# Optimization experiments

Measured on AMD Instinct MI355X. Metric: run time of the kernel, lower is better.

The kernel has to match this reference:

```python
import jax, jax.numpy as jnp
import numpy as np
from jax import lax

NDF = 128
OUT_CH = 256
N_INPUT = 4096
H = W = 64
A_FEAT = OUT_CH * 2 * 2   # 1024
B_OUT = OUT_CH            # 256
C_ROW = 16
BATCH = 128
EPS = 1e-5


def conv2d_s2(x, w):
    # x: NCHW, w: OIHW, stride 2, pad 1 (kernel 4) -> halves spatial dims
    return lax.conv_general_dilated(x, w, window_strides=(2, 2),
                                    padding=[(1, 1), (1, 1)],
                                    dimension_numbers=("NCHW", "OIHW", "NCHW"))


def batchnorm(x, gamma, beta):
    # training-mode batch stats over (N, H, W)
    mean = jnp.mean(x, axis=(0, 2, 3), keepdims=True)
    var = jnp.var(x, axis=(0, 2, 3), keepdims=True)
    xn = (x - mean) * lax.rsqrt(var + EPS)
    return xn * gamma[None, :, None, None] + beta[None, :, None, None]


def lrelu(x):
    return jnp.where(x >= 0, x, 0.2 * x)


def setup_inputs() -> dict:
    key = jax.random.key(0)
    ks = jax.random.split(key, 16)
    s = lambda fan: 1.0 / np.sqrt(fan)
    inp = {
        "image": jax.random.normal(ks[0], (BATCH, 3, H, W), jnp.float32),
        "word_vectors": jax.random.normal(ks[1], (BATCH, N_INPUT), jnp.float32),
        "fc_w": jax.random.normal(ks[2], (H * W, N_INPUT), jnp.float32) * s(N_INPUT),
        "w1": jax.random.normal(ks[3], (NDF, 4, 4, 4), jnp.float32) * s(4 * 16),
        "w2": jax.random.normal(ks[4], (NDF * 2, NDF, 4, 4), jnp.float32) * s(NDF * 16),
        "w3": jax.random.normal(ks[5], (NDF * 2, NDF * 2, 4, 4), jnp.float32) * s(NDF * 2 * 16),
        "w4": jax.random.normal(ks[6], (NDF * 4, NDF * 2, 4, 4), jnp.float32) * s(NDF * 2 * 16),
        "w5": jax.random.normal(ks[7], (OUT_CH, NDF * 4, 4, 4), jnp.float32) * s(NDF * 4 * 16),
        "g2": jnp.ones((NDF * 2,), jnp.float32),
        "b2": jnp.zeros((NDF * 2,), jnp.float32),
        "g3": jnp.ones((NDF * 2,), jnp.float32),
        "b3": jnp.zeros((NDF * 2,), jnp.float32),
        "g4": jnp.ones((NDF * 4,), jnp.float32),
        "b4": jnp.zeros((NDF * 4,), jnp.float32),
        "T": jax.random.uniform(ks[8], (A_FEAT, B_OUT, C_ROW), jnp.float32,
                                 minval=0.0, maxval=1.0 / A_FEAT),
    }
    return inp


def reference(image, word_vectors, fc_w, w1, w2, w3, w4, w5,
              g2, b2, g3, b3, g4, b4, T):
    b = image.shape[0]
    # fc: Linear(no bias) + ReLU (dropout = identity at p=0 / eval)
    wv = jax.nn.relu(word_vectors @ fc_w.T)            # [b, H*W]
    wv = wv.reshape(b, 1, H, W)
    x = jnp.concatenate([image, wv], axis=1)           # [b, 4, 64, 64]
    # conv stack (spectral norm acts on weights; raw weights used here)
    x = lrelu(conv2d_s2(x, w1))                        # [b, ndf, 32, 32]
    x = lrelu(batchnorm(conv2d_s2(x, w2), g2, b2))     # [b, 2ndf, 16, 16]
    x = lrelu(batchnorm(conv2d_s2(x, w3), g3, b3))     # [b, 2ndf, 8, 8]
    x = lrelu(batchnorm(conv2d_s2(x, w4), g4, b4))     # [b, 4ndf, 4, 4]
    x = conv2d_s2(x, w5)                               # [b, out_ch, 2, 2]
    # minibatch discrimination
    feat = x.reshape(b, A_FEAT)                        # [b, 1024]
    Ms = (feat @ T.reshape(A_FEAT, B_OUT * C_ROW)).reshape(b, B_OUT, C_ROW)
    # pairwise L1 over C, exp, sum over batch (including self, as in the loop)
    d = jnp.sum(jnp.abs(Ms[:, None, :, :] - Ms[None, :, :, :]), axis=-1)  # [b,b,B]
    mbd = jnp.sum(jnp.exp(-d), axis=1)                 # [b, B]
    return jnp.concatenate([feat, mbd], axis=1)        # [b, 1280]
```

## Files before the change

kernel.cpp:

```cpp
#include <hip/hip_runtime.h>
#include <cstddef>

#define BB 128

typedef unsigned short u16;
typedef __attribute__((ext_vector_type(8))) short short8;
typedef __attribute__((ext_vector_type(4))) short short4v;
typedef __attribute__((ext_vector_type(4))) float f32x4;

constexpr int ilog2c(int v){ return v<=1 ? 0 : 1+ilog2c(v>>1); }

__device__ __forceinline__ u16 f2b(float f){
  union {float f; unsigned u;} x; x.f = f;
  unsigned u = x.u + 0x7fffu + ((x.u>>16)&1u);
  return (u16)(u>>16);
}
__device__ __forceinline__ float b2f(u16 h){
  union {unsigned u; float f;} x; x.u = ((unsigned)h)<<16;
  return x.f;
}

#define GLOAD_LDS16(gsrc, ldsdst) \
  __builtin_amdgcn_global_load_lds((const __attribute__((address_space(1))) void*)(gsrc), \
      (__attribute__((address_space(3))) void*)(ldsdst), 16, 0, 0)

template<int IC, int OC, int OH, int STORE, int KSPLIT=1>
__global__ __launch_bounds__(512) void convmm2(
    const u16* __restrict__ xp, const u16* __restrict__ wtT, void* __restrict__ yv)
{
  constexpr int OW = OH, S = OH*OW;
  constexpr int IHp = 2*OH+2, IWp = 2*OW+2;
  constexpr int KT = 16*IC;
  constexpr int KTS = KT / KSPLIT;
  constexpr int NT = KTS / 64;
  constexpr int LS = ilog2c(S), LOW = ilog2c(OW), L4 = ilog2c(4*IC);
  __shared__ u16 As[2*128*64];
  __shared__ u16 Bs[2*128*64];
  const int tid = threadIdx.x;
  const int m0 = blockIdx.x*128;
  const int n0 = blockIdx.y*128;
  const int kbase = (KSPLIT>1) ? blockIdx.z*KTS : 0;
  const int wave = tid>>6, l = tid&63;
  const int wm = wave>>1, wn = wave&1;

  size_t abase[2]; int au[2];
  #pragma unroll
  for (int t=0;t<2;++t){
    int unit = tid + t*512;
    int r = unit>>3, us = unit&7;
    au[t] = us ^ (r&7);
    int p = m0 + r;
    int b = p >> LS, s = p & (S-1);
    int oh = s >> LOW, ow = s & (OW-1);
    abase[t] = ((size_t)(b*IHp + 2*oh)*IWp + 2*ow)*IC;
  }
  const u16* bsrc[2];
  #pragma unroll
  for (int t=0;t<2;++t){
    int unit = tid + t*512;
    int r = unit>>3, us = unit&7;
    bsrc[t] = wtT + (size_t)(n0+r)*KT + (size_t)(us ^ (r&7))*8;
  }

  auto stage = [&](int half, int k0){
    #pragma unroll
    for (int t=0;t<2;++t){
      int k = k0 + au[t]*8;
      int kh = k >> L4, koff = k & (4*IC-1);
      GLOAD_LDS16(xp + abase[t] + (size_t)kh*IWp*IC + koff,
                  &As[half*8192 + (size_t)(t*512 + wave*64)*8]);
    }
    #pragma unroll
    for (int t=0;t<2;++t){
      GLOAD_LDS16(bsrc[t] + k0, &Bs[half*8192 + (size_t)(t*512 + wave*64)*8]);
    }
  };

  f32x4 acc[2][4] = {};

  stage(0, kbase);
  __syncthreads();
  int cur = 0;
  for (int t=0; t<NT; ++t){
    if (t+1 < NT) stage(cur^1, kbase + (t+1)*64);
    #pragma unroll
    for (int kk=0;kk<2;++kk){
      short8 af[2], bfm[4];
      #pragma unroll
      for (int mi=0;mi<2;++mi){
        int row = wm*32 + mi*16 + (l&15);
        int u = (kk*4 + (l>>4)) ^ (row&7);
        af[mi] = *(const short8*)(&As[cur*8192 + row*64 + u*8]);
      }
      #pragma unroll
      for (int ni=0;ni<4;++ni){
        int row = wn*64 + ni*16 + (l&15);
        int u = (kk*4 + (l>>4)) ^ (row&7);
        bfm[ni] = *(const short8*)(&Bs[cur*8192 + row*64 + u*8]);
      }
      #pragma unroll
      for (int mi=0;mi<2;++mi)
        #pragma unroll
        for (int ni=0;ni<4;++ni)
          acc[mi][ni] = __builtin_amdgcn_mfma_f32_16x16x32_bf16(af[mi], bfm[ni], acc[mi][ni], 0,0,0);
    }
    __syncthreads();
    cur ^= 1;
  }
  #pragma unroll
  for (int mi=0;mi<2;++mi){
    #pragma unroll
    for (int ni=0;ni<4;++ni){
      #pragma unroll
      for (int r=0;r<4;++r){
        int row = m0 + wm*32 + mi*16 + (l>>4)*4 + r;
        int col = n0 + wn*64 + ni*16 + (l&15);
        float v = acc[mi][ni][r];
        if (STORE==0){
          ((u16*)yv)[(size_t)row*OC + col] = f2b(v);
        } else if (STORE==1){
          v = v>=0.f ? v : 0.2f*v;
          int b = row>>LS, s = row&(S-1);
          int oh = s>>LOW, ow = s&(OW-1);
          ((u16*)yv)[((size_t)(b*(OH+2) + oh+1)*(OW+2) + ow+1)*OC + col] = f2b(v);
        } else {
          ((float*)yv)[((size_t)blockIdx.z*(BB*S) + row)*OC + col] = v;
        }
      }
    }
  }
}

template<int B_FP32>
__global__ __launch_bounds__(256) void gemm128_split(
    const u16* __restrict__ A, const void* __restrict__ Bsrc,
    float* __restrict__ part, int K, int kchunk)
{
  __shared__ u16 As[2*128*64];
  __shared__ u16 Bs[2*64*64];
  const int tid = threadIdx.x;
  const int n0 = blockIdx.x*64;
  const int kbase = blockIdx.y*kchunk;
  const int wave = tid>>6, l = tid&63;
  const u16* asrc[4];
  #pragma unroll
  for (int t=0;t<4;++t){
    int unit = tid + t*256, r = unit>>3, us = unit&7;
    asrc[t] = A + (size_t)r*K + (size_t)(us ^ (r&7))*8;
  }
  const float* bf32[4]; int bdst32[4];
  const u16* b16[2];
  if (B_FP32){
    const float* Bf = (const float*)Bsrc;
    #pragma unroll
    for (int t=0;t<4;++t){
      int unit = tid + t*256;
      int r = unit>>4, u4 = unit&15;
      int u = u4>>1, hf = u4&1;
      int us = u ^ (r&7);
      bf32[t] = Bf + (size_t)(n0+r)*K + u4*4;
      bdst32[t] = r*64 + us*8 + hf*4;
    }
  } else {
    const u16* Bb = (const u16*)Bsrc;
    #pragma unroll
    for (int t=0;t<2;++t){
      int unit = tid + t*256, r = unit>>3, us = unit&7;
      b16[t] = Bb + (size_t)(n0+r)*K + (size_t)(us ^ (r&7))*8;
    }
  }

  auto stageA = [&](int half, int k0){
    #pragma unroll
    for (int t=0;t<4;++t)
      GLOAD_LDS16(asrc[t] + k0, &As[half*8192 + (size_t)(t*256 + wave*64)*8]);
  };
  auto stageB16 = [&](int half, int k0){
    #pragma unroll
    for (int t=0;t<2;++t)
      GLOAD_LDS16(b16[t] + k0, &Bs[half*4096 + (size_t)(t*256 + wave*64)*8]);
  };
  float4 breg[4];
  auto loadB32 = [&](int k0){
    #pragma unroll
    for (int t=0;t<4;++t) breg[t] = *(const float4*)(bf32[t] + k0);
  };
  auto writeB32 = [&](int half){
    #pragma unroll
    for (int t=0;t<4;++t){
      short4v o; o[0]=(short)f2b(breg[t].x); o[1]=(short)f2b(breg[t].y);
      o[2]=(short)f2b(breg[t].z); o[3]=(short)f2b(breg[t].w);
      *(short4v*)(&Bs[half*4096 + bdst32[t]]) = o;
    }
  };

  f32x4 acc[2][4] = {};
  const int NT = kchunk >> 6;
  stageA(0, kbase);
  if (B_FP32){ loadB32(kbase); writeB32(0); } else stageB16(0, kbase);
  __syncthreads();
  int cur = 0;
  for (int t=0;t<NT;++t){
    const int k0 = kbase + t*64;
    if (t+1 < NT){
      stageA(cur^1, k0+64);
      if (B_FP32) loadB32(k0+64);
      else stageB16(cur^1, k0+64);
    }
    #pragma unroll
    for (int kk=0;kk<2;++kk){
      short8 af[2], bfm[4];
      #pragma unroll
      for (int mi=0;mi<2;++mi){
        int row = wave*32 + mi*16 + (l&15);
        int u = (kk*4 + (l>>4)) ^ (row&7);
        af[mi] = *(const short8*)(&As[cur*8192 + row*64 + u*8]);
      }
      #pragma unroll
      for (int ni=0;ni<4;++ni){
        int row = ni*16 + (l&15);
        int u = (kk*4 + (l>>4)) ^ (row&7);
        bfm[ni] = *(const short8*)(&Bs[cur*4096 + row*64 + u*8]);
      }
      #pragma unroll
      for (int mi=0;mi<2;++mi)
        #pragma unroll
        for (int ni=0;ni<4;++ni)
          acc[mi][ni] = __builtin_amdgcn_mfma_f32_16x16x32_bf16(af[mi], bfm[ni], acc[mi][ni], 0,0,0);
    }
    if (B_FP32 && t+1 < NT) writeB32(cur^1);
    __syncthreads();
    cur ^= 1;
  }
  #pragma unroll
  for (int mi=0;mi<2;++mi){
    #pragma unroll
    for (int ni=0;ni<4;++ni){
      #pragma unroll
      for (int r=0;r<4;++r){
        int m = wave*32 + mi*16 + (l>>4)*4 + r;
        int n = n0 + ni*16 + (l&15);
        part[((size_t)blockIdx.y*128 + m)*4096 + n] = acc[mi][ni][r];
      }
    }
  }
}

template<int Hp, int C>
__device__ __forceinline__ void zb_border(u16* __restrict__ buf, int idx, int count){
  if (idx >= count) return;
  constexpr int NP = 4*Hp - 4;
  constexpr int PC = NP*C;
  int b = idx / PC;
  int rem = idx - b*PC;
  int p = rem >> ilog2c(C);
  int c = rem & (C-1);
  int h, w;
  if (p < Hp){ h = 0; w = p; }
  else if (p < 2*Hp){ h = Hp-1; w = p - Hp; }
  else { int q = p - 2*Hp; h = 1 + (q>>1); w = (q&1) ? (Hp-1) : 0; }
  buf[(((size_t)b*Hp + h)*Hp + w)*C + c] = 0;
}

__global__ __launch_bounds__(256) void fc_reduce_zb(const float* __restrict__ part,
                                                    u16* __restrict__ xp0,
                                                    u16* __restrict__ xp1, u16* __restrict__ xp2)
{
  const int blk = blockIdx.x, tid = threadIdx.x;
  if (blk < 2048){
    int idx = blk*256 + tid;
    float s = 0.f;
    #pragma unroll
    for (int i=0;i<16;++i) s += part[(size_t)i*524288 + idx];
    float v = fmaxf(s, 0.f);
    int m = idx>>12, n = idx&4095;
    int h = n>>6, w2 = n&63;
    xp0[((size_t)(m*66 + h+1)*66 + w2+1)*4 + 3] = f2b(v);
  } else if (blk < 10496){
    zb_border<34,128>(xp1, (blk-2048)*256 + tid, 2162688);
  } else {
    zb_border<18,256>(xp2, (blk-10496)*256 + tid, 2228224);
  }
}

__global__ __launch_bounds__(256) void reduce_ms(const float* __restrict__ part, float* __restrict__ outv)
{
  int idx = blockIdx.x*256 + threadIdx.x;
  float s = 0.f;
  #pragma unroll
  for (int i=0;i<8;++i) s += part[(size_t)i*524288 + idx];
  outv[idx] = s;
}

template<int NS, int C>
__global__ __launch_bounds__(256) void reduce_bn(
    const float* __restrict__ part, u16* __restrict__ y,
    float* __restrict__ stats, int Mblk, int Mtot)
{
  constexpr int CU = C/8, NR = 256/CU, LCU = ilog2c(CU);
  __shared__ float red[NR*C];
  const int cu = threadIdx.x & (CU-1);
  const int rg = threadIdx.x >> LCU;
  const int base = blockIdx.x*Mblk;
  float s[8] = {}, ss[8] = {};
  for (int p = base+rg; p < base+Mblk; p += NR){
    float a8[8];
    #pragma unroll
    for (int j=0;j<8;++j) a8[j]=0.f;
    #pragma unroll
    for (int i=0;i<NS;++i){
      const float* src = part + ((size_t)i*Mtot + p)*C + cu*8;
      float4 v0 = *(const float4*)src;
      float4 v1 = *(const float4*)(src+4);
      a8[0]+=v0.x; a8[1]+=v0.y; a8[2]+=v0.z; a8[3]+=v0.w;
      a8[4]+=v1.x; a8[5]+=v1.y; a8[6]+=v1.z; a8[7]+=v1.w;
    }
    u16 o[8];
    #pragma unroll
    for (int j=0;j<8;++j){
      o[j] = f2b(a8[j]);
      float vb = b2f(o[j]);
      s[j]+=vb; ss[j]+=vb*vb;
    }
    *(short8*)(y + (size_t)p*C + cu*8) = *(short8*)o;
  }
  #pragma unroll
  for (int j=0;j<8;++j) red[rg*C + cu*8 + j] = s[j];
  __syncthreads();
  for (int c=threadIdx.x; c<C; c+=256){
    float t=0.f;
    #pragma unroll
    for (int r2=0;r2<NR;++r2) t += red[r2*C+c];
    stats[blockIdx.x*512 + c] = t;
  }
  __syncthreads();
  #pragma unroll
  for (int j=0;j<8;++j) red[rg*C + cu*8 + j] = ss[j];
  __syncthreads();
  for (int c=threadIdx.x; c<C; c+=256){
    float t=0.f;
    #pragma unroll
    for (int r2=0;r2<NR;++r2) t += red[r2*C+c];
    stats[131072 + blockIdx.x*512 + c] = t;
  }
}

__global__ __launch_bounds__(256) void conv5_reduce(const float* __restrict__ part,
                                                    float* __restrict__ out, u16* __restrict__ featb)
{
  int idx = blockIdx.x*256 + threadIdx.x;
  float s = 0.f;
  #pragma unroll
  for (int i=0;i<32;++i) s += part[(size_t)i*131072 + idx];
  int row = idx>>8, col = idx&255;
  int b = row>>2, sp = row&3;
  out[(size_t)b*1280 + col*4 + sp] = s;
  featb[(size_t)b*1024 + col*4 + sp] = f2b(s);
}

template<int IC, int ICP>
__device__ __forceinline__ void repack_dev(const float* __restrict__ w, u16* __restrict__ wt,
                                           int oc, int tid, float* ls){
  for (int i=tid; i<IC*16; i+=256){
    int ic = i>>4, khkw = i&15;
    ls[ic*17+khkw] = w[(size_t)oc*IC*16 + i];
  }
  __syncthreads();
  constexpr int KT = 16*ICP;
  constexpr int LP = ilog2c(ICP);
  for (int k=tid; k<KT; k+=256){
    int khkw = k >> LP, ic = k & (ICP-1);
    float v = (ic<IC) ? ls[ic*17+khkw] : 0.f;
    wt[(size_t)oc*KT + k] = f2b(v);
  }
}

__device__ __forceinline__ void transpose_dev(const float* __restrict__ T, u16* __restrict__ Tt,
                                              int idx, int tid, float* tile){
  int bx = idx & 127, by = idx >> 7;
  int kb = by*32, nb = bx*32;
  int tx = tid&31, ty = tid>>5;
  #pragma unroll
  for (int i=0;i<32;i+=8)
    tile[(ty+i)*33 + tx] = T[(size_t)(kb+ty+i)*4096 + nb+tx];
  __syncthreads();
  #pragma unroll
  for (int i=0;i<32;i+=8)
    Tt[(size_t)(nb+ty+i)*1024 + kb+tx] = f2b(tile[tx*33 + ty+i]);
}

__global__ __launch_bounds__(256) void prep_all(
    const float* __restrict__ w1, const float* __restrict__ w2, const float* __restrict__ w3,
    const float* __restrict__ w4, const float* __restrict__ w5, const float* __restrict__ T,
    const float* __restrict__ wvec, const float* __restrict__ img,
    u16* wt1T, u16* wt2T, u16* wt3T, u16* wt4T, u16* wt5T, u16* Tt, u16* wvb, u16* xp0)
{
  __shared__ float ls[512*17];
  const int blk = blockIdx.x, tid = threadIdx.x;
  if (blk < 128)        repack_dev<4,4>(w1, wt1T, blk, tid, ls);
  else if (blk < 384)   repack_dev<128,128>(w2, wt2T, blk-128, tid, ls);
  else if (blk < 640)   repack_dev<256,256>(w3, wt3T, blk-384, tid, ls);
  else if (blk < 1152)  repack_dev<256,256>(w4, wt4T, blk-640, tid, ls);
  else if (blk < 1408)  repack_dev<512,512>(w5, wt5T, blk-1152, tid, ls);
  else if (blk < 5504)  transpose_dev(T, Tt, blk-1408, tid, ls);
  else if (blk < 7552){ int i = (blk-5504)*256 + tid; wvb[i] = f2b(wvec[i]); }
  else if (blk < 9600){
    int idx = (blk-7552)*256 + tid;
    int b = idx>>12, s = idx&4095;
    int h = s>>6, w = s&63;
    short4v o;
    o[0] = (short)f2b(img[(size_t)(b*3+0)*4096 + s]);
    o[1] = (short)f2b(img[(size_t)(b*3+1)*4096 + s]);
    o[2] = (short)f2b(img[(size_t)(b*3+2)*4096 + s]);
    o[3] = 0;
    *(short4v*)(xp0 + ((size_t)(b*66 + h+1)*66 + w+1)*4) = o;
  } else {
    zb_border<66,4>(xp0, (blk-9600)*256 + tid, 133120);
  }
}

template<int C>
__global__ __launch_bounds__(256) void bn_stats2(const u16* __restrict__ y, float* __restrict__ stats, int Mblk){
  constexpr int CU = C/8, NR = 256/CU, LCU = ilog2c(CU);
  __shared__ float red[NR*C];
  const int cu = threadIdx.x & (CU-1);
  const int rg = threadIdx.x >> LCU;
  const int base = blockIdx.x*Mblk;
  float s[8] = {}, ss[8] = {};
  for (int p = base+rg; p < base+Mblk; p += NR){
    short8 v = *(const short8*)(y + (size_t)p*C + cu*8);
    #pragma unroll
    for (int j=0;j<8;++j){ float f=b2f((u16)v[j]); s[j]+=f; ss[j]+=f*f; }
  }
  #pragma unroll
  for (int j=0;j<8;++j) red[rg*C + cu*8 + j] = s[j];
  __syncthreads();
  for (int c=threadIdx.x; c<C; c+=256){
    float t=0.f;
    #pragma unroll
    for (int r2=0;r2<NR;++r2) t += red[r2*C+c];
    stats[blockIdx.x*512 + c] = t;
  }
  __syncthreads();
  #pragma unroll
  for (int j=0;j<8;++j) red[rg*C + cu*8 + j] = ss[j];
  __syncthreads();
  for (int c=threadIdx.x; c<C; c+=256){
    float t=0.f;
    #pragma unroll
    for (int r2=0;r2<NR;++r2) t += red[r2*C+c];
    stats[131072 + blockIdx.x*512 + c] = t;
  }
}

template<int C>
__global__ __launch_bounds__(C) void bn_finalize(float* __restrict__ stats, const float* __restrict__ g,
                                                 const float* __restrict__ be, float cnt){
  int c = threadIdx.x;
  float s=0.f, ss=0.f;
  for (int b=0;b<256;++b){ s += stats[b*512+c]; ss += stats[131072 + b*512+c]; }
  float m = s/cnt;
  float var = ss/cnt - m*m;
  float A = rsqrtf(var + 1e-5f)*g[c];
  stats[262144 + c] = A;
  stats[262144 + 512 + c] = be[c] - m*A;
}

template<int C, int OH>
__device__ __forceinline__ void bn_apply_body(const u16* __restrict__ y, const float* __restrict__ stats,
                                              u16* __restrict__ xp, int idx){
  constexpr int S = OH*OH, LS = ilog2c(S), LOW = ilog2c(OH);
  constexpr int CU = C/8, LCU = ilog2c(CU);
  int p = idx >> LCU, cu = idx & (CU-1);
  short8 v8 = *(const short8*)(y + (size_t)p*C + cu*8);
  const float* Ap = stats + 262144;
  const float* Bp = stats + 262144 + 512;
  u16 o[8];
  #pragma unroll
  for (int j=0;j<8;++j){
    float v = b2f((u16)v8[j])*Ap[cu*8+j] + Bp[cu*8+j];
    o[j] = f2b(v>=0.f ? v : 0.2f*v);
  }
  int b = p>>LS, s = p&(S-1), oh = s>>LOW, ow = s&(OH-1);
  *(short8*)(xp + ((size_t)(b*(OH+2)+oh+1)*(OH+2)+ow+1)*C + cu*8) = *(short8*)o;
}

template<int C, int OH>
__global__ __launch_bounds__(256) void bn_apply(const u16* __restrict__ y, const float* __restrict__ stats,
                                                u16* __restrict__ xp){
  bn_apply_body<C,OH>(y, stats, xp, blockIdx.x*256 + threadIdx.x);
}

__global__ __launch_bounds__(256) void bn_apply2_zb(const u16* __restrict__ y, const float* __restrict__ stats,
                                                    u16* __restrict__ xp, u16* xp3, u16* xp4){
  const int blk = blockIdx.x, tid = threadIdx.x;
  if (blk < 4096)       bn_apply_body<256,16>(y, stats, xp, blk*256 + tid);
  else if (blk < 8704)  zb_border<10,256>(xp3, (blk-4096)*256 + tid, 1179648);
  else                  zb_border<6,512>(xp4, (blk-8704)*256 + tid, 1310720);
}

__global__ __launch_bounds__(256) void mbd_part(const float* __restrict__ Ms, float* __restrict__ part)
{
  const int i = blockIdx.x;
  const int ch = blockIdx.y;
  const int o = threadIdx.x;
  float mi[16];
  #pragma unroll
  for (int u = 0; u < 4; ++u) {
    float4 v = *(const float4*)&Ms[(size_t)i * 4096 + o * 16 + u * 4];
    mi[u*4+0]=v.x; mi[u*4+1]=v.y; mi[u*4+2]=v.z; mi[u*4+3]=v.w;
  }
  float acc = 0.f;
  for (int j = ch*16; j < ch*16 + 16; ++j) {
    float d = 0.f;
    #pragma unroll
    for (int u = 0; u < 4; ++u) {
      float4 v = *(const float4*)&Ms[(size_t)j * 4096 + o * 16 + u * 4];
      d += fabsf(mi[u*4+0]-v.x) + fabsf(mi[u*4+1]-v.y) + fabsf(mi[u*4+2]-v.z) + fabsf(mi[u*4+3]-v.w);
    }
    acc += __expf(-d);
  }
  part[((size_t)ch*128 + i)*256 + o] = acc;
}

__global__ __launch_bounds__(256) void mbd_reduce(const float* __restrict__ part, float* __restrict__ out)
{
  int idx = blockIdx.x*256 + threadIdx.x;
  int i = idx>>8, o = idx&255;
  float s = 0.f;
  #pragma unroll
  for (int c=0;c<8;++c) s += part[((size_t)c*128 + i)*256 + o];
  out[(size_t)i*1280 + 1024 + o] = s;
}

__global__ void ws_too_small(float* out, int n){
  int idx = blockIdx.x*256+threadIdx.x;
  if (idx<n) out[idx] = -777.0f;
}

extern "C" void kernel_launch(void* const* d_in, const int* in_sizes, int n_in,
                              void* d_out, int out_size, void* d_ws, size_t ws_size,
                              hipStream_t stream)
{
  const float* image = (const float*)d_in[0];
  const float* wvec  = (const float*)d_in[1];
  const float* fc_w  = (const float*)d_in[2];
  const float* w1    = (const float*)d_in[3];
  const float* w2    = (const float*)d_in[4];
  const float* w3    = (const float*)d_in[5];
  const float* w4    = (const float*)d_in[6];
  const float* w5    = (const float*)d_in[7];
  const float* g2    = (const float*)d_in[8];
  const float* b2    = (const float*)d_in[9];
  const float* g3    = (const float*)d_in[10];
  const float* b3    = (const float*)d_in[11];
  const float* g4    = (const float*)d_in[12];
  const float* b4    = (const float*)d_in[13];
  const float* T     = (const float*)d_in[14];
  float* out = (float*)d_out;
  char* wsb = (char*)d_ws;

  const size_t NEED = 105816064ull;
  if (ws_size < NEED) {
    ws_too_small<<<(out_size + 255)/256, 256, 0, stream>>>(out, out_size);
    return;
  }

  u16* xp1   = (u16*)(wsb + 0);
  u16* y3    = (u16*)(wsb + 0);
  u16* xp3   = (u16*)(wsb + 4194304);
  u16* y4    = (u16*)(wsb + 10747904);
  u16* xp4   = (u16*)(wsb + 12845056);
  float* Ms  = (float*)(wsb + 17563648);
  u16* featb = (u16*)(wsb + 19660800);
  float* stats = (float*)(wsb + 19922944);
  u16* xp2   = (u16*)(wsb + 37879808);
  float* gpartF = (float*)(wsb + 37879808);
  float* c4part = (float*)(wsb + 37879808);
  float* c5part = (float*)(wsb + 37879808);
  float* mbdpart = (float*)(wsb + 37879808);
  u16* y2    = (u16*)(wsb + 59113472);
  float* gpartM = (float*)(wsb + 59113472);
  float* c3part = (float*)(wsb + 59113472);
  u16* xp0   = (u16*)(wsb + 75890688);
  u16* wt1T  = (u16*)(wsb + 84811776);
  u16* wt2T  = (u16*)(wsb + 84844544);
  u16* wt3T  = (u16*)(wsb + 85893120);
  u16* wt4T  = (u16*)(wsb + 87990272);
  u16* wt5T  = (u16*)(wsb + 92184576);
  u16* Tt    = (u16*)(wsb + 96378880);
  u16* wvb   = (u16*)(wsb + 104767488);

  prep_all<<<10120, 256, 0, stream>>>(w1, w2, w3, w4, w5, T, wvec, image,
                                      wt1T, wt2T, wt3T, wt4T, wt5T, Tt, wvb, xp0);

  gemm128_split<1><<<dim3(64,16), 256, 0, stream>>>(wvb, fc_w, gpartF, 4096, 256);
  fc_reduce_zb<<<19200, 256, 0, stream>>>(gpartF, xp0, xp1, xp2);

  convmm2<4,128,32,1><<<dim3(1024,1), 512, 0, stream>>>(xp0, wt1T, xp1);
  convmm2<128,256,16,0><<<dim3(256,2), 512, 0, stream>>>(xp1, wt2T, y2);

  bn_stats2<256><<<256, 256, 0, stream>>>(y2, stats, 128);
  bn_finalize<256><<<1, 256, 0, stream>>>(stats, g2, b2, 32768.f);
  bn_apply2_zb<<<13824, 256, 0, stream>>>(y2, stats, xp2, xp3, xp4);

  convmm2<256,256,8,3,2><<<dim3(64,2,2), 512, 0, stream>>>(xp2, wt3T, c3part);
  reduce_bn<2,256><<<256, 256, 0, stream>>>(c3part, y3, stats, 32, 8192);
  bn_finalize<256><<<1, 256, 0, stream>>>(stats, g3, b3, 8192.f);
  bn_apply<256,8><<<1024, 256, 0, stream>>>(y3, stats, xp3);

  convmm2<256,512,4,3,4><<<dim3(16,4,4), 512, 0, stream>>>(xp3, wt4T, c4part);
  reduce_bn<4,512><<<256, 256, 0, stream>>>(c4part, y4, stats, 8, 2048);
  bn_finalize<512><<<1, 512, 0, stream>>>(stats, g4, b4, 2048.f);
  bn_apply<512,4><<<512, 256, 0, stream>>>(y4, stats, xp4);

  convmm2<512,256,2,3,32><<<dim3(4,2,32), 512, 0, stream>>>(xp4, wt5T, c5part);
  conv5_reduce<<<512, 256, 0, stream>>>(c5part, out, featb);

  gemm128_split<0><<<dim3(64,8), 256, 0, stream>>>(featb, Tt, gpartM, 1024, 128);
  reduce_ms<<<2048, 256, 0, stream>>>(gpartM, Ms);

  mbd_part<<<dim3(128,8), 256, 0, stream>>>(Ms, mbdpart);
  mbd_reduce<<<128, 256, 0, stream>>>(mbdpart, out);
}
```

Before: 266.9 us.

## Store split-K partials in bf16 and fuse minibatch-discrimination reduction

Split-K partial sums from the fc GEMM and conv3/4/5 are written and read as bf16 instead of fp32, halving the traffic of these intermediate buffers. The two-kernel minibatch-discrimination part/reduce is merged into one kernel with 1024-thread blocks reducing through shared memory, removing a launch and a global round trip. Rounding partials to bf16 before summation adds accumulation error.

```diff
diff --git a/kernel.cpp b/kernel.cpp
--- a/kernel.cpp
+++ b/kernel.cpp
@@ -124,17 +124,17 @@
           int oh = s>>LOW, ow = s&(OW-1);
           ((u16*)yv)[((size_t)(b*(OH+2) + oh+1)*(OW+2) + ow+1)*OC + col] = f2b(v);
         } else {
-          ((float*)yv)[((size_t)blockIdx.z*(BB*S) + row)*OC + col] = v;
+          ((u16*)yv)[((size_t)blockIdx.z*(BB*S) + row)*OC + col] = f2b(v);
         }
       }
     }
   }
 }
 
-template<int B_FP32>
+template<int B_FP32, int P16>
 __global__ __launch_bounds__(256) void gemm128_split(
     const u16* __restrict__ A, const void* __restrict__ Bsrc,
-    float* __restrict__ part, int K, int kchunk)
+    void* __restrict__ part, int K, int kchunk)
 {
   __shared__ u16 As[2*128*64];
   __shared__ u16 Bs[2*64*64];
@@ -240,7 +240,9 @@
       for (int r=0;r<4;++r){
         int m = wave*32 + mi*16 + (l>>4)*4 + r;
         int n = n0 + ni*16 + (l&15);
-        part[((size_t)blockIdx.y*128 + m)*4096 + n] = acc[mi][ni][r];
+        size_t off = ((size_t)blockIdx.y*128 + m)*4096 + n;
+        if (P16) ((u16*)part)[off] = f2b(acc[mi][ni][r]);
+        else     ((float*)part)[off] = acc[mi][ni][r];
       }
     }
   }
@@ -262,7 +264,7 @@
   buf[(((size_t)b*Hp + h)*Hp + w)*C + c] = 0;
 }
 
-__global__ __launch_bounds__(256) void fc_reduce_zb(const float* __restrict__ part,
+__global__ __launch_bounds__(256) void fc_reduce_zb(const u16* __restrict__ part,
                                                     u16* __restrict__ xp0,
                                                     u16* __restrict__ xp1, u16* __restrict__ xp2)
 {
@@ -271,7 +273,7 @@
     int idx = blk*256 + tid;
     float s = 0.f;
     #pragma unroll
-    for (int i=0;i<16;++i) s += part[(size_t)i*524288 + idx];
+    for (int i=0;i<16;++i) s += b2f(part[(size_t)i*524288 + idx]);
     float v = fmaxf(s, 0.f);
     int m = idx>>12, n = idx&4095;
     int h = n>>6, w2 = n&63;
@@ -294,7 +296,7 @@
 
 template<int NS, int C>
 __global__ __launch_bounds__(256) void reduce_bn(
-    const float* __restrict__ part, u16* __restrict__ y,
+    const u16* __restrict__ part, u16* __restrict__ y,
     float* __restrict__ stats, int Mblk, int Mtot)
 {
   constexpr int CU = C/8, NR = 256/CU, LCU = ilog2c(CU);
@@ -309,11 +311,9 @@
     for (int j=0;j<8;++j) a8[j]=0.f;
     #pragma unroll
     for (int i=0;i<NS;++i){
-      const float* src = part + ((size_t)i*Mtot + p)*C + cu*8;
-      float4 v0 = *(const float4*)src;
-      float4 v1 = *(const float4*)(src+4);
-      a8[0]+=v0.x; a8[1]+=v0.y; a8[2]+=v0.z; a8[3]+=v0.w;
-      a8[4]+=v1.x; a8[5]+=v1.y; a8[6]+=v1.z; a8[7]+=v1.w;
+      short8 v = *(const short8*)(part + ((size_t)i*Mtot + p)*C + cu*8);
+      #pragma unroll
+      for (int j=0;j<8;++j) a8[j] += b2f((u16)v[j]);
     }
     u16 o[8];
     #pragma unroll
@@ -345,13 +345,13 @@
   }
 }
 
-__global__ __launch_bounds__(256) void conv5_reduce(const float* __restrict__ part,
+__global__ __launch_bounds__(256) void conv5_reduce(const u16* __restrict__ part,
                                                     float* __restrict__ out, u16* __restrict__ featb)
 {
   int idx = blockIdx.x*256 + threadIdx.x;
   float s = 0.f;
   #pragma unroll
-  for (int i=0;i<32;++i) s += part[(size_t)i*131072 + idx];
+  for (int i=0;i<32;++i) s += b2f(part[(size_t)i*131072 + idx]);
   int row = idx>>8, col = idx&255;
   int b = row>>2, sp = row&3;
   out[(size_t)b*1280 + col*4 + sp] = s;
@@ -499,11 +499,12 @@
   else                  zb_border<6,512>(xp4, (blk-8704)*256 + tid, 1310720);
 }
 
-__global__ __launch_bounds__(256) void mbd_part(const float* __restrict__ Ms, float* __restrict__ part)
-{
+__global__ __launch_bounds__(1024) void mbd_fused(const float* __restrict__ Ms, float* __restrict__ out)
+{
+  __shared__ float red[4][256];
   const int i = blockIdx.x;
-  const int ch = blockIdx.y;
-  const int o = threadIdx.x;
+  const int o = threadIdx.x & 255;
+  const int jg = threadIdx.x >> 8;
   float mi[16];
   #pragma unroll
   for (int u = 0; u < 4; ++u) {
@@ -511,7 +512,7 @@
     mi[u*4+0]=v.x; mi[u*4+1]=v.y; mi[u*4+2]=v.z; mi[u*4+3]=v.w;
   }
   float acc = 0.f;
-  for (int j = ch*16; j < ch*16 + 16; ++j) {
+  for (int j = jg*32; j < jg*32 + 32; ++j) {
     float d = 0.f;
     #pragma unroll
     for (int u = 0; u < 4; ++u) {
@@ -520,17 +521,10 @@
     }
     acc += __expf(-d);
   }
-  part[((size_t)ch*128 + i)*256 + o] = acc;
-}
-
-__global__ __launch_bounds__(256) void mbd_reduce(const float* __restrict__ part, float* __restrict__ out)
-{
-  int idx = blockIdx.x*256 + threadIdx.x;
-  int i = idx>>8, o = idx&255;
-  float s = 0.f;
-  #pragma unroll
-  for (int c=0;c<8;++c) s += part[((size_t)c*128 + i)*256 + o];
-  out[(size_t)i*1280 + 1024 + o] = s;
+  red[jg][o] = acc;
+  __syncthreads();
+  if (jg == 0)
+    out[(size_t)i*1280 + 1024 + o] = red[0][o] + red[1][o] + red[2][o] + red[3][o];
 }
 
 __global__ void ws_too_small(float* out, int n){
@@ -575,13 +569,12 @@
   u16* featb = (u16*)(wsb + 19660800);
   float* stats = (float*)(wsb + 19922944);
   u16* xp2   = (u16*)(wsb + 37879808);
-  float* gpartF = (float*)(wsb + 37879808);
-  float* c4part = (float*)(wsb + 37879808);
-  float* c5part = (float*)(wsb + 37879808);
-  float* mbdpart = (float*)(wsb + 37879808);
+  u16* c4part = (u16*)(wsb + 37879808);
+  u16* c5part = (u16*)(wsb + 37879808);
   u16* y2    = (u16*)(wsb + 59113472);
+  u16* gpartF = (u16*)(wsb + 59113472);
   float* gpartM = (float*)(wsb + 59113472);
-  float* c3part = (float*)(wsb + 59113472);
+  u16* c3part = (u16*)(wsb + 59113472);
   u16* xp0   = (u16*)(wsb + 75890688);
   u16* wt1T  = (u16*)(wsb + 84811776);
   u16* wt2T  = (u16*)(wsb + 84844544);
@@ -594,7 +587,7 @@
   prep_all<<<10120, 256, 0, stream>>>(w1, w2, w3, w4, w5, T, wvec, image,
                                       wt1T, wt2T, wt3T, wt4T, wt5T, Tt, wvb, xp0);
 
-  gemm128_split<1><<<dim3(64,16), 256, 0, stream>>>(wvb, fc_w, gpartF, 4096, 256);
+  gemm128_split<1,1><<<dim3(64,16), 256, 0, stream>>>(wvb, fc_w, gpartF, 4096, 256);
   fc_reduce_zb<<<19200, 256, 0, stream>>>(gpartF, xp0, xp1, xp2);
 
   convmm2<4,128,32,1><<<dim3(1024,1), 512, 0, stream>>>(xp0, wt1T, xp1);
@@ -617,9 +610,8 @@
   convmm2<512,256,2,3,32><<<dim3(4,2,32), 512, 0, stream>>>(xp4, wt5T, c5part);
   conv5_reduce<<<512, 256, 0, stream>>>(c5part, out, featb);
 
-  gemm128_split<0><<<dim3(64,8), 256, 0, stream>>>(featb, Tt, gpartM, 1024, 128);
+  gemm128_split<0,0><<<dim3(64,8), 256, 0, stream>>>(featb, Tt, gpartM, 1024, 128);
   reduce_ms<<<2048, 256, 0, stream>>>(gpartM, Ms);
 
-  mbd_part<<<dim3(128,8), 256, 0, stream>>>(Ms, mbdpart);
-  mbd_reduce<<<128, 256, 0, stream>>>(mbdpart, out);
-}
+  mbd_fused<<<128, 1024, 0, stream>>>(Ms, out);
+}
```

New measurement: 268.7 us. About the same (+0.7%).
